# Kernel optimization log

Hardware: AMD Instinct MI355X
Metric: run time of the kernel (lower is better)

## Reference

```python
import jax, jax.numpy as jnp
import numpy as np


def setup_inputs() -> dict:
    key = jax.random.key(0)
    ks = jax.random.split(key, 5)
    B, H, W, KV = 32, 32, 32, 1024
    N, K, V = 16, 64, 64
    return {
        "key_value": jax.random.normal(ks[0], (B, H, W, KV), dtype=jnp.float32),
        "query": jax.random.normal(ks[1], (1, 1, N, K), dtype=jnp.float32),
        "k_kernel": jax.random.normal(ks[2], (KV, N * K), dtype=jnp.float32) * 0.03,
        "k_bias": jnp.zeros((N * K,), dtype=jnp.float32),
        "v_kernel": jax.random.normal(ks[3], (KV, N * V), dtype=jnp.float32) * 0.03,
        "v_bias": jnp.zeros((N * V,), dtype=jnp.float32),
    }


def reference(key_value, query, k_kernel, k_bias, v_kernel, v_bias):
    # key_value: [B,H,W,KV]; 1x1 conv == channel GEMM
    B, H, W, KV = key_value.shape
    N, K = query.shape[2], query.shape[3]
    V = v_kernel.shape[1] // N
    x = key_value.reshape(B, H * W, KV)                      # [B,HW,KV]
    k = (x @ k_kernel + k_bias).reshape(B, H * W, N, K)       # [B,HW,N,K]
    v = (x @ v_kernel + v_bias).reshape(B, H * W, N, V)       # [B,HW,N,V]
    # single-query dot product per head (no 1/sqrt(K) scaling, per original)
    logits = jnp.einsum('bsnk,nk->bsn', k, query[0, 0])       # [B,HW,N]
    attn = jax.nn.softmax(logits, axis=1)                     # softmax over HW
    out = jnp.einsum('bsn,bsnv->bnv', attn, v)                # [B,N,V]
    return out
```

## Files before the change

kernel.cpp:

```cpp
#include <hip/hip_runtime.h>
#include <hip/hip_fp16.h>


typedef _Float16 f16x8 __attribute__((ext_vector_type(8)));
typedef float f32x4 __attribute__((ext_vector_type(4)));

__device__ __forceinline__ float rlane(float v, int l) {
  return __int_as_float(__builtin_amdgcn_readlane(__float_as_int(v), l));
}

__global__ __launch_bounds__(256) void k_qk(const float* __restrict__ kk,
                                            const float* __restrict__ q,
                                            const float* __restrict__ kb,
                                            __half* __restrict__ qkb,
                                            float* __restrict__ qb) {
  const int gid = blockIdx.x * 256 + threadIdx.x;
  const int c = gid >> 4, n = gid & 15;
  float a = 0.f;
#pragma unroll
  for (int k4 = 0; k4 < 64; k4 += 4) {
    const float4 kv = *(const float4*)(kk + (size_t)c * 1024 + n * 64 + k4);
    const float4 qv = *(const float4*)(q + n * 64 + k4);
    a += kv.x * qv.x + kv.y * qv.y + kv.z * qv.z + kv.w * qv.w;
  }
  const int kbi = c >> 5;
  const int l = (((c >> 3) & 3) << 4) | n;
  const int j = c & 7;
  qkb[kbi * 512 + l * 8 + j] = __float2half(a);
  if (blockIdx.x == 0 && threadIdx.x < 16) {
    float s = 0.f;
    for (int k = 0; k < 64; k++) s += kb[threadIdx.x * 64 + k] * q[threadIdx.x * 64 + k];
    qb[threadIdx.x] = s;
  }
}

__global__ __launch_bounds__(512, 4) void k_fused(const float* __restrict__ x,
                                                  const __half* __restrict__ qkb,
                                                  const float* __restrict__ qb,
                                                  float* __restrict__ mch,
                                                  float* __restrict__ lch,
                                                  __half* __restrict__ wph) {
  __shared__ __half qkt[16384];
  __shared__ float et2[64 * 17 + 4];
  const int tid = threadIdx.x;
  const int lane = tid & 63;
  const int wid = tid >> 6;
  const int blk = blockIdx.x;
  const int srow0 = blk * 64;

#pragma unroll
  for (int it = 0; it < 4; ++it) {
    const int g = it * 512 + tid;
    ((uint4*)qkt)[g] = ((const uint4*)qkb)[g];
  }
  __syncthreads();

  {
    const int wtile = wid & 3;
    const int khalf = wid >> 2;
    const int r16 = lane & 15;
    const int khi = lane >> 4;
    const float* xg = x + (size_t)(srow0 + wtile * 16 + r16) * 1024
                        + khalf * 512 + khi * 8;
    const __half* qbase = qkt + (khalf * 16) * 512 + lane * 8;

    f32x4 dacc = {0.f, 0.f, 0.f, 0.f};
    float4 pa0 = *(const float4*)(xg);
    float4 pa1 = *(const float4*)(xg + 4);
    float4 pb0, pb1;

#pragma unroll 1
    for (int kbs = 0; kbs < 16; kbs += 2) {
      pb0 = *(const float4*)(xg + (kbs + 1) * 32);
      pb1 = *(const float4*)(xg + (kbs + 1) * 32 + 4);
      {
        f16x8 af;
        af[0] = (_Float16)pa0.x; af[1] = (_Float16)pa0.y;
        af[2] = (_Float16)pa0.z; af[3] = (_Float16)pa0.w;
        af[4] = (_Float16)pa1.x; af[5] = (_Float16)pa1.y;
        af[6] = (_Float16)pa1.z; af[7] = (_Float16)pa1.w;
        const f16x8 bf = *(const f16x8*)(qbase + kbs * 512);
        dacc = __builtin_amdgcn_mfma_f32_16x16x32_f16(af, bf, dacc, 0, 0, 0);
      }
      if (kbs + 2 < 16) {
        pa0 = *(const float4*)(xg + (kbs + 2) * 32);
        pa1 = *(const float4*)(xg + (kbs + 2) * 32 + 4);
      }
      {
        f16x8 af;
        af[0] = (_Float16)pb0.x; af[1] = (_Float16)pb0.y;
        af[2] = (_Float16)pb0.z; af[3] = (_Float16)pb0.w;
        af[4] = (_Float16)pb1.x; af[5] = (_Float16)pb1.y;
        af[6] = (_Float16)pb1.z; af[7] = (_Float16)pb1.w;
        const f16x8 bf = *(const f16x8*)(qbase + (kbs + 1) * 512);
        dacc = __builtin_amdgcn_mfma_f32_16x16x32_f16(af, bf, dacc, 0, 0, 0);
      }
    }

    const float qbv = qb[r16];
    if (khalf == 0) {
#pragma unroll
      for (int reg = 0; reg < 4; ++reg)
        et2[(wtile * 16 + khi * 4 + reg) * 17 + r16] = dacc[reg] + qbv;
    }
    __syncthreads();
    if (khalf == 1) {
#pragma unroll
      for (int reg = 0; reg < 4; ++reg)
        et2[(wtile * 16 + khi * 4 + reg) * 17 + r16] += dacc[reg];
    }
    __syncthreads();
  }

#pragma unroll
  for (int t = 0; t < 2; ++t) {
    const int nn = wid + t * 8;
    const float v = et2[lane * 17 + nn];
    float m = v;
#pragma unroll
    for (int d = 1; d < 64; d <<= 1) m = fmaxf(m, __shfl_xor(m, d));
    const float e = __expf(v - m);
    float s = e;
#pragma unroll
    for (int d = 1; d < 64; d <<= 1) s += __shfl_xor(s, d);
    if (lane == 0) {
      mch[blk * 16 + nn] = m;
      lch[blk * 16 + nn] = s;
    }
    et2[lane * 17 + nn] = e;
  }
  __syncthreads();

  {
    const int c0 = tid * 2;
    float acc0[16], acc1[16];
#pragma unroll
    for (int n = 0; n < 16; ++n) { acc0[n] = 0.f; acc1[n] = 0.f; }
    const float* xp = x + (size_t)srow0 * 1024 + c0;

    float  ea = et2[(lane >> 4) * 17 + (lane & 15)];
    float2 xca[4];
#pragma unroll
    for (int ss = 0; ss < 4; ++ss) xca[ss] = *(const float2*)(xp + (size_t)ss * 1024);

#pragma unroll 1
    for (int sg = 0; sg < 16; ++sg) {
      float  eb = 0.f;
      float2 xcb[4];
      if (sg < 15) {
        const int s0n = (sg + 1) * 4;
        eb = et2[(s0n + (lane >> 4)) * 17 + (lane & 15)];
#pragma unroll
        for (int ss = 0; ss < 4; ++ss)
          xcb[ss] = *(const float2*)(xp + (size_t)(s0n + ss) * 1024);
      }
#pragma unroll
      for (int ss = 0; ss < 4; ++ss) {
#pragma unroll
        for (int n = 0; n < 16; ++n) {
          const float ev = rlane(ea, ss * 16 + n);
          acc0[n] += ev * xca[ss].x;
          acc1[n] += ev * xca[ss].y;
        }
      }
      ea = eb;
#pragma unroll
      for (int ss = 0; ss < 4; ++ss) xca[ss] = xcb[ss];
    }

    __half* wpp = wph + (size_t)blk * 16384;
#pragma unroll
    for (int n = 0; n < 16; ++n) {
      __half2 h = __floats2half2_rn(acc0[n], acc1[n]);
      *(__half2*)(wpp + n * 1024 + c0) = h;
    }
  }
}

__global__ __launch_bounds__(256) void k_out(const __half* __restrict__ wph,
                                             const float* __restrict__ vk,
                                             const float* __restrict__ vb,
                                             const float* __restrict__ mch,
                                             const float* __restrict__ lch,
                                             float* __restrict__ out) {
  const int bi = blockIdx.x;
  const int b = bi >> 4, n = bi & 15;
  const int tid = threadIdx.x;
  __shared__ float wrow[1024];
  __shared__ float red[4][64];

  float m16[16], l16[16];
#pragma unroll
  for (int ch = 0; ch < 16; ++ch) {
    m16[ch] = mch[(b * 16 + ch) * 16 + n];
    l16[ch] = lch[(b * 16 + ch) * 16 + n];
  }
  float mg = m16[0];
#pragma unroll
  for (int ch = 1; ch < 16; ++ch) mg = fmaxf(mg, m16[ch]);
  float fac[16], lg = 0.f;
#pragma unroll
  for (int ch = 0; ch < 16; ++ch) { fac[ch] = __expf(m16[ch] - mg); lg += fac[ch] * l16[ch]; }

  float4 a4 = {0.f, 0.f, 0.f, 0.f};
#pragma unroll
  for (int ch = 0; ch < 16; ch++) {
    const __half2* p = (const __half2*)(wph + ((size_t)(b * 16 + ch) * 16 + n) * 1024 + tid * 4);
    const float2 f01 = __half22float2(p[0]);
    const float2 f23 = __half22float2(p[1]);
    a4.x += fac[ch] * f01.x; a4.y += fac[ch] * f01.y;
    a4.z += fac[ch] * f23.x; a4.w += fac[ch] * f23.y;
  }
  *(float4*)&wrow[tid * 4] = a4;
  __syncthreads();

  const int v = tid & 63, cq = tid >> 6;
  float a = 0.f;
  const float* vkc = vk + n * 64 + v;
  for (int ci = 0; ci < 256; ci++) {
    const int c = cq * 256 + ci;
    a += wrow[c] * vkc[(size_t)c * 1024];
  }
  red[cq][v] = a;
  __syncthreads();
  if (tid < 64) {
    const float o = (red[0][tid] + red[1][tid] + red[2][tid] + red[3][tid]) / lg
                    + vb[n * 64 + tid];
    out[(size_t)b * 1024 + n * 64 + tid] = o;
  }
}

extern "C" void kernel_launch(void* const* d_in, const int* in_sizes, int n_in,
                              void* d_out, int out_size, void* d_ws, size_t ws_size,
                              hipStream_t stream) {
  const float* x  = (const float*)d_in[0];
  const float* q  = (const float*)d_in[1];
  const float* kk = (const float*)d_in[2];
  const float* kb = (const float*)d_in[3];
  const float* vk = (const float*)d_in[4];
  const float* vb = (const float*)d_in[5];
  float* out = (float*)d_out;

  float*  f   = (float*)d_ws;
  __half* qkb = (__half*)f;
  float*  qb  = f + 8192;
  float*  mch = f + 8208;
  float*  lch = f + 16400;
  __half* wph = (__half*)(f + 24592);

  hipLaunchKernelGGL(k_qk,    dim3(64),  dim3(256), 0, stream, kk, q, kb, qkb, qb);
  hipLaunchKernelGGL(k_fused, dim3(512), dim3(512), 0, stream, x, qkb, qb, mch, lch, wph);
  hipLaunchKernelGGL(k_out,   dim3(512), dim3(256), 0, stream, wph, vk, vb, mch, lch, out);
}
```

Before: 66.98 us.

## Double k_fused block to 1024 threads, splitting K and rows across more waves

k_fused now launches 1024 threads per block. The logits MFMA loop is split four ways over the K dimension, with two shared partial tiles summed during the softmax. The weighted-sum phase splits the 64 rows into two halves whose fp16 partials are combined through an extra 32KB shared buffer. Each wave now handles one head in softmax instead of two. The goal is more waves per block to hide memory latency, at the cost of extra shared memory, extra barriers, an fp16 rounding of the partial sum, and likely lower blocks-per-CU occupancy.

Measured after the change: 68.06 us. No clear change (+1.6%).

```diff
diff --git a/kernel.cpp b/kernel.cpp
--- a/kernel.cpp
+++ b/kernel.cpp
@@ -34,14 +34,16 @@
   }
 }
 
-__global__ __launch_bounds__(512, 4) void k_fused(const float* __restrict__ x,
-                                                  const __half* __restrict__ qkb,
-                                                  const float* __restrict__ qb,
-                                                  float* __restrict__ mch,
-                                                  float* __restrict__ lch,
-                                                  __half* __restrict__ wph) {
+__global__ __launch_bounds__(1024, 8) void k_fused(const float* __restrict__ x,
+                                                   const __half* __restrict__ qkb,
+                                                   const float* __restrict__ qb,
+                                                   float* __restrict__ mch,
+                                                   float* __restrict__ lch,
+                                                   __half* __restrict__ wph) {
   __shared__ __half qkt[16384];
+  __shared__ __half ovl[16384];
   __shared__ float et2[64 * 17 + 4];
+  __shared__ float etB[64 * 17 + 4];
   const int tid = threadIdx.x;
   const int lane = tid & 63;
   const int wid = tid >> 6;
@@ -49,20 +51,20 @@
   const int srow0 = blk * 64;
 
 #pragma unroll
-  for (int it = 0; it < 4; ++it) {
-    const int g = it * 512 + tid;
+  for (int it = 0; it < 2; ++it) {
+    const int g = it * 1024 + tid;
     ((uint4*)qkt)[g] = ((const uint4*)qkb)[g];
   }
   __syncthreads();
 
   {
     const int wtile = wid & 3;
-    const int khalf = wid >> 2;
+    const int kq = wid >> 2;
     const int r16 = lane & 15;
     const int khi = lane >> 4;
     const float* xg = x + (size_t)(srow0 + wtile * 16 + r16) * 1024
-                        + khalf * 512 + khi * 8;
-    const __half* qbase = qkt + (khalf * 16) * 512 + lane * 8;
+                        + kq * 256 + khi * 8;
+    const __half* qbase = qkt + kq * 4096 + lane * 8;
 
     f32x4 dacc = {0.f, 0.f, 0.f, 0.f};
     float4 pa0 = *(const float4*)(xg);
@@ -70,7 +72,7 @@
     float4 pb0, pb1;
 
 #pragma unroll 1
-    for (int kbs = 0; kbs < 16; kbs += 2) {
+    for (int kbs = 0; kbs < 8; kbs += 2) {
       pb0 = *(const float4*)(xg + (kbs + 1) * 32);
       pb1 = *(const float4*)(xg + (kbs + 1) * 32 + 4);
       {
@@ -82,7 +84,7 @@
         const f16x8 bf = *(const f16x8*)(qbase + kbs * 512);
         dacc = __builtin_amdgcn_mfma_f32_16x16x32_f16(af, bf, dacc, 0, 0, 0);
       }
-      if (kbs + 2 < 16) {
+      if (kbs + 2 < 8) {
         pa0 = *(const float4*)(xg + (kbs + 2) * 32);
         pa1 = *(const float4*)(xg + (kbs + 2) * 32 + 4);
       }
@@ -97,25 +99,28 @@
       }
     }
 
-    const float qbv = qb[r16];
-    if (khalf == 0) {
-#pragma unroll
-      for (int reg = 0; reg < 4; ++reg)
-        et2[(wtile * 16 + khi * 4 + reg) * 17 + r16] = dacc[reg] + qbv;
+    const int erow = wtile * 16 + khi * 4;
+    if (kq == 0) {
+#pragma unroll
+      for (int reg = 0; reg < 4; ++reg) et2[(erow + reg) * 17 + r16] = dacc[reg];
+    } else if (kq == 2) {
+#pragma unroll
+      for (int reg = 0; reg < 4; ++reg) etB[(erow + reg) * 17 + r16] = dacc[reg];
     }
     __syncthreads();
-    if (khalf == 1) {
-#pragma unroll
-      for (int reg = 0; reg < 4; ++reg)
-        et2[(wtile * 16 + khi * 4 + reg) * 17 + r16] += dacc[reg];
+    if (kq == 1) {
+#pragma unroll
+      for (int reg = 0; reg < 4; ++reg) et2[(erow + reg) * 17 + r16] += dacc[reg];
+    } else if (kq == 3) {
+#pragma unroll
+      for (int reg = 0; reg < 4; ++reg) etB[(erow + reg) * 17 + r16] += dacc[reg];
     }
     __syncthreads();
   }
 
-#pragma unroll
-  for (int t = 0; t < 2; ++t) {
-    const int nn = wid + t * 8;
-    const float v = et2[lane * 17 + nn];
+  {
+    const int nn = wid;
+    const float v = et2[lane * 17 + nn] + etB[lane * 17 + nn] + qb[nn];
     float m = v;
 #pragma unroll
     for (int d = 1; d < 64; d <<= 1) m = fmaxf(m, __shfl_xor(m, d));
@@ -132,24 +137,27 @@
   __syncthreads();
 
   {
-    const int c0 = tid * 2;
+    const int sgrp = tid >> 9;
+    const int tl = tid & 511;
+    const int c0 = tl * 2;
+    const int sb = sgrp * 32;
     float acc0[16], acc1[16];
 #pragma unroll
     for (int n = 0; n < 16; ++n) { acc0[n] = 0.f; acc1[n] = 0.f; }
-    const float* xp = x + (size_t)srow0 * 1024 + c0;
-
-    float  ea = et2[(lane >> 4) * 17 + (lane & 15)];
+    const float* xp = x + (size_t)(srow0 + sb) * 1024 + c0;
+
+    float  ea = et2[(sb + (lane >> 4)) * 17 + (lane & 15)];
     float2 xca[4];
 #pragma unroll
     for (int ss = 0; ss < 4; ++ss) xca[ss] = *(const float2*)(xp + (size_t)ss * 1024);
 
 #pragma unroll 1
-    for (int sg = 0; sg < 16; ++sg) {
+    for (int sg = 0; sg < 8; ++sg) {
       float  eb = 0.f;
       float2 xcb[4];
-      if (sg < 15) {
+      if (sg < 7) {
         const int s0n = (sg + 1) * 4;
-        eb = et2[(s0n + (lane >> 4)) * 17 + (lane & 15)];
+        eb = et2[(sb + s0n + (lane >> 4)) * 17 + (lane & 15)];
 #pragma unroll
         for (int ss = 0; ss < 4; ++ss)
           xcb[ss] = *(const float2*)(xp + (size_t)(s0n + ss) * 1024);
@@ -168,11 +176,20 @@
       for (int ss = 0; ss < 4; ++ss) xca[ss] = xcb[ss];
     }
 
-    __half* wpp = wph + (size_t)blk * 16384;
-#pragma unroll
-    for (int n = 0; n < 16; ++n) {
-      __half2 h = __floats2half2_rn(acc0[n], acc1[n]);
-      *(__half2*)(wpp + n * 1024 + c0) = h;
+    if (sgrp == 1) {
+#pragma unroll
+      for (int n = 0; n < 16; ++n)
+        *(__half2*)(ovl + n * 1024 + c0) = __floats2half2_rn(acc0[n], acc1[n]);
+    }
+    __syncthreads();
+    if (sgrp == 0) {
+      __half* wpp = wph + (size_t)blk * 16384;
+#pragma unroll
+      for (int n = 0; n < 16; ++n) {
+        const float2 o = __half22float2(*(const __half2*)(ovl + n * 1024 + c0));
+        *(__half2*)(wpp + n * 1024 + c0) =
+            __floats2half2_rn(acc0[n] + o.x, acc1[n] + o.y);
+      }
     }
   }
 }
@@ -248,7 +265,7 @@
   float*  lch = f + 16400;
   __half* wph = (__half*)(f + 24592);
 
-  hipLaunchKernelGGL(k_qk,    dim3(64),  dim3(256), 0, stream, kk, q, kb, qkb, qb);
-  hipLaunchKernelGGL(k_fused, dim3(512), dim3(512), 0, stream, x, qkb, qb, mch, lch, wph);
-  hipLaunchKernelGGL(k_out,   dim3(512), dim3(256), 0, stream, wph, vk, vb, mch, lch, out);
-}
+  hipLaunchKernelGGL(k_qk,    dim3(64),  dim3(256),  0, stream, kk, q, kb, qkb, qb);
+  hipLaunchKernelGGL(k_fused, dim3(512), dim3(1024), 0, stream, x, qkb, qb, mch, lch, wph);
+  hipLaunchKernelGGL(k_out,   dim3(512), dim3(256),  0, stream, wph, vk, vb, mch, lch, out);
+}
```
